# Optimization experiments

Hardware: AMD Instinct MI355X
Metric: run time of the kernel (lower is better)

## Reference

```python
import jax, jax.numpy as jnp
import numpy as np

LN_EPS = 1e-5
NEG_INF = -1e30


def setup_inputs() -> dict:
    key = jax.random.key(0)
    k_adj, k_feat, k_mask, k_w = jax.random.split(key, 4)
    B, N, H, R, L = 8, 400, 768, 46, 2
    adj = jax.random.uniform(k_adj, (B, N, N, R), dtype=jnp.float32)
    feature = jax.random.normal(k_feat, (B, N, H), dtype=jnp.float32)
    dmask = (jax.random.uniform(k_mask, (B, 1, N)) > 0.1).astype(jnp.float32)
    # per-layer, per-relation Linear(H, H, bias=False) weights, applied as x @ W
    W = jax.random.normal(k_w, (L, R, H, H), dtype=jnp.float32) / np.sqrt(H)
    return {"adj": adj, "feature": feature, "dmask": dmask, "W": W}


def reference(adj, feature, dmask, W):
    # adj: [B,N,N,R] -> [B,R,N,N]; dmask: [B,1,N] masks key/column axis
    B, N, _, R = adj.shape
    a = jnp.transpose(adj, (0, 3, 1, 2))           # [B,R,N,N]
    m = dmask[:, None, :, :]                        # [B,1,1,N]
    logits = a * m + (1.0 - m) * NEG_INF
    att = jax.nn.softmax(logits, axis=-1)           # [B,R,N,N] (layer-invariant)

    x = feature
    num_layers = W.shape[0]
    for layer in range(num_layers):
        # grouped per-relation linear: h[b,r,n,k] = feature[b,n,h] @ W[layer,r,h,k]
        h = jnp.einsum('bnh,rhk->brnk', x, W[layer])
        h = jax.nn.relu(jnp.einsum('brnm,brmk->brnk', att, h))
        addition = h.sum(axis=1)                    # sum over relations -> [B,N,H]
        z = jax.nn.relu(addition) / R
        # LayerNorm without affine params
        mu = jnp.mean(z, axis=-1, keepdims=True)
        var = jnp.var(z, axis=-1, keepdims=True)
        x = (z - mu) / jnp.sqrt(var + LN_EPS)
        # dropout is identity in eval mode
    return x
```

## Files before the change

### kernel.cpp

```cpp
#include <hip/hip_runtime.h>
#include <stdint.h>

#define BS 8
#define NN 400
#define HH 768
#define RR 46
#define MPAD 416
#define MFLAT2 3328
#define LDW2 3328
#define PADM 402

typedef _Float16 half8 __attribute__((ext_vector_type(8)));
typedef _Float16 half4v __attribute__((ext_vector_type(4)));
typedef float floatx4 __attribute__((ext_vector_type(4)));

__device__ __forceinline__ void async16(const void* g, void* l) {
  __builtin_amdgcn_global_load_lds((const __attribute__((address_space(1))) uint32_t*)g,
                                   (__attribute__((address_space(3))) uint32_t*)l, 16, 0, 0);
}

__device__ __forceinline__ int xcd_work(int flat, int nwg) {
  int q = nwg >> 3, rem = nwg & 7;
  int xcd = flat & 7, slot = flat >> 3;
  return (xcd < rem ? xcd * (q + 1) : rem * (q + 1) + (xcd - rem) * q) + slot;
}

__device__ __forceinline__ void vm_wait(int ahead) {
  if (ahead >= 2) asm volatile("s_waitcnt vmcnt(8)" ::: "memory");
  else if (ahead == 1) asm volatile("s_waitcnt vmcnt(4)" ::: "memory");
  else asm volatile("s_waitcnt vmcnt(0)" ::: "memory");
}
__device__ __forceinline__ void vm_wait2(int ahead) {
  if (ahead >= 2) asm volatile("s_waitcnt vmcnt(4)" ::: "memory");
  else if (ahead == 1) asm volatile("s_waitcnt vmcnt(2)" ::: "memory");
  else asm volatile("s_waitcnt vmcnt(0)" ::: "memory");
}
#define BAR_TOP() { __builtin_amdgcn_s_barrier(); __builtin_amdgcn_sched_barrier(0); }
#define BAR_BOT() { asm volatile("s_waitcnt lgkmcnt(0)" ::: "memory"); \
                    __builtin_amdgcn_s_barrier(); __builtin_amdgcn_sched_barrier(0); }
#define BAR_ONE() { asm volatile("s_barrier" ::: "memory"); __builtin_amdgcn_sched_barrier(0); }


__device__ __forceinline__ void stage_tile(const _Float16* __restrict__ g, int ld, int rowbase,
                                           int maxrow, int kbase, _Float16* lds, int t) {
  int w = t >> 6, lane = t & 63;
  int swz = ((lane & 3) ^ ((lane >> 3) & 3)) * 8;
#pragma unroll
  for (int j = 0; j < 2; ++j) {
    int chunk = w * 2 + j;
    int row = chunk * 16 + (lane >> 2);
    int grow = rowbase + row;
    grow = grow > maxrow ? maxrow : grow;
    async16(g + (size_t)grow * ld + kbase + swz, lds + chunk * 512);
  }
}

__device__ __forceinline__ void mma_tiles(const _Float16* As, const _Float16* Bs, int lane,
                                          int wr, int wc, floatx4 acc[4][4]) {
  int arow = wr + (lane & 15);
  int brow = wc + (lane & 15);
  int kswz = ((lane >> 4) ^ ((lane >> 1) & 3)) * 8;
  half8 a[4], b[4];
#pragma unroll
  for (int i = 0; i < 4; ++i) a[i] = *(const half8*)&As[(arow + i * 16) * 32 + kswz];
#pragma unroll
  for (int i = 0; i < 4; ++i) b[i] = *(const half8*)&Bs[(brow + i * 16) * 32 + kswz];
#pragma unroll
  for (int i = 0; i < 4; ++i)
#pragma unroll
    for (int j = 0; j < 4; ++j)
      acc[i][j] = __builtin_amdgcn_mfma_f32_16x16x32_f16(a[i], b[j], acc[i][j], 0, 0, 0);
}

__device__ __forceinline__ void mma8(const _Float16* As, const _Float16* Bs, int lane,
                                     int wr, int wc, floatx4 acc[4][2]) {
  int arow = wr + (lane & 15);
  int brow = wc + (lane & 15);
  int kswz = ((lane >> 4) ^ ((lane >> 1) & 3)) * 8;
  half8 a[4], b[2];
#pragma unroll
  for (int i = 0; i < 4; ++i) a[i] = *(const half8*)&As[(arow + i * 16) * 32 + kswz];
#pragma unroll
  for (int j = 0; j < 2; ++j) b[j] = *(const half8*)&Bs[(brow + j * 16) * 32 + kswz];
#pragma unroll
  for (int i = 0; i < 4; ++i)
#pragma unroll
    for (int j = 0; j < 2; ++j)
      acc[i][j] = __builtin_amdgcn_mfma_f32_16x16x32_f16(a[i], b[j], acc[i][j], 0, 0, 0);
}

__global__ __launch_bounds__(256) void conv_w(const float* __restrict__ W, _Float16* __restrict__ Wt) {
  __shared__ float tl[32][33];
  int t = threadIdx.x;
  int lr = blockIdx.y;
  int tr = blockIdx.x / 24, tc = blockIdx.x % 24;
  const float* src = W + (size_t)lr * HH * HH;
  _Float16* dst = Wt + (size_t)lr * HH * HH;
  int rl = t >> 5, cl = t & 31;
#pragma unroll
  for (int j = 0; j < 4; ++j)
    tl[rl + 8 * j][cl] = src[(size_t)(tr * 32 + rl + 8 * j) * HH + tc * 32 + cl];
  __syncthreads();
#pragma unroll
  for (int j = 0; j < 4; ++j)
    dst[(size_t)(tc * 32 + rl + 8 * j) * HH + tr * 32 + cl] = (_Float16)tl[cl][rl + 8 * j];
}

__global__ void conv_x(const float* __restrict__ f, _Float16* __restrict__ x16) {
  int i4 = blockIdx.x * 256 + threadIdx.x;
  int row = i4 / 192;
  int c4 = i4 - row * 192;
  int b = row / 416;
  int m = row - b * 416;
  half4v h = {};
  if (m < NN) {
    float4 v = *(const float4*)(f + ((size_t)(b * NN + m) * HH) + c4 * 4);
    h[0] = (_Float16)v.x; h[1] = (_Float16)v.y; h[2] = (_Float16)v.z; h[3] = (_Float16)v.w;
  }
  *(half4v*)&x16[(size_t)row * HH + c4 * 4] = h;
}

__global__ __launch_bounds__(512) void att_softmax(const float* __restrict__ adj,
                                                   const float* __restrict__ dmask,
                                                   _Float16* __restrict__ att) {
  __shared__ _Float16 sE[RR * PADM];
  __shared__ float sM[NN];
  int t = threadIdx.x;
  int n = blockIdx.x, b = blockIdx.y;
  const float4* src = (const float4*)(adj + ((size_t)b * NN + n) * NN * RR);
  for (int i = t; i < NN; i += 512) sM[i] = dmask[b * NN + i];
  float4 v[9];
#pragma unroll
  for (int k = 0; k < 9; ++k) {
    int idx = t + k * 512;
    if (idx < NN * RR / 4) v[k] = src[idx];
  }
  __syncthreads();
#pragma unroll
  for (int k = 0; k < 9; ++k) {
    int idx = t + k * 512;
    if (idx < NN * RR / 4) {
      int e0 = idx * 4;
      float vv[4] = {v[k].x, v[k].y, v[k].z, v[k].w};
#pragma unroll
      for (int j = 0; j < 4; ++j) {
        int e = e0 + j;
        int m = e / RR;
        int r = e - m * RR;
        float val = sM[m] > 0.5f ? __expf(vv[j]) : 0.0f;
        sE[r * PADM + m] = (_Float16)val;
      }
    }
  }
  __syncthreads();
  int lane = t & 63, wid = t >> 6;
  for (int r = wid; r < RR; r += 8) {
    const _Float16* row = &sE[r * PADM];
    float s = 0.f;
    for (int m = lane; m < NN; m += 64) s += (float)row[m];
#pragma unroll
    for (int o = 32; o; o >>= 1) s += __shfl_xor(s, o);
    float inv = 1.0f / s;
    _Float16* orow = att + (((size_t)b * RR + r) * NN + n) * MPAD;
    for (int m2 = lane * 2; m2 < MPAD; m2 += 128) {
      _Float16 lo = (_Float16)0.f, hi = (_Float16)0.f;
      if (m2 < NN) lo = (_Float16)((float)row[m2] * inv);
      if (m2 + 1 < NN) hi = (_Float16)((float)row[m2 + 1] * inv);
      union { _Float16 h[2]; uint32_t u; } pk;
      pk.h[0] = lo; pk.h[1] = hi;
      *(uint32_t*)&orow[m2] = pk.u;
    }
  }
}

__global__ __launch_bounds__(256) void gemm_xw(const _Float16* __restrict__ x16,
                                               const _Float16* __restrict__ Wt,
                                               _Float16* __restrict__ h1T, int layer, int r0, int rbase) {
  __shared__ __align__(16) char smraw[49152];
  int t = threadIdx.x;
  int work = xcd_work(blockIdx.x, gridDim.x);
  int r_i = work / 156;
  int rem = work - r_i * 156;
  int r = r0 + r_i;
  int mtile = rem / 6, ntile = rem % 6;
  const _Float16* A = x16;
  const _Float16* Bp = Wt + ((size_t)layer * RR + r) * HH * HH;
  int lane = t & 63, w = t >> 6;
  int wr = (w >> 1) * 64, wc = (w & 1) * 64;
  floatx4 acc[4][4] = {};
  stage_tile(A, HH, mtile * 128, MFLAT2 - 1, 0, (_Float16*)smraw, t);
  stage_tile(Bp, HH, ntile * 128, HH - 1, 0, (_Float16*)(smraw + 8192), t);
  stage_tile(A, HH, mtile * 128, MFLAT2 - 1, 32, (_Float16*)(smraw + 16384), t);
  stage_tile(Bp, HH, ntile * 128, HH - 1, 32, (_Float16*)(smraw + 24576), t);
  int cur = 0, stb = 2;
  for (int ks = 0; ks < 24; ++ks) {
    if (ks + 2 < 24) {
      char* nb = smraw + stb * 16384;
      stage_tile(A, HH, mtile * 128, MFLAT2 - 1, (ks + 2) * 32, (_Float16*)nb, t);
      stage_tile(Bp, HH, ntile * 128, HH - 1, (ks + 2) * 32, (_Float16*)(nb + 8192), t);
      stb = stb == 2 ? 0 : stb + 1;
    }
    vm_wait(ks + 2 < 24 ? 2 : (ks + 1 < 24 ? 1 : 0));
    BAR_TOP();
    char* cb = smraw + cur * 16384;
    mma_tiles((const _Float16*)cb, (const _Float16*)(cb + 8192), lane, wr, wc, acc);
    BAR_BOT();
    cur = cur == 2 ? 0 : cur + 1;
  }
  _Float16* outl = (_Float16*)smraw;
#pragma unroll
  for (int i = 0; i < 4; ++i) {
#pragma unroll
    for (int j = 0; j < 4; ++j) {
      int rl = wr + i * 16 + (lane >> 4) * 4;
      int cl = wc + j * 16 + (lane & 15);
      half4v v = {(_Float16)acc[i][j][0], (_Float16)acc[i][j][1],
                  (_Float16)acc[i][j][2], (_Float16)acc[i][j][3]};
      *(half4v*)&outl[cl * 136 + rl] = v;
    }
  }
  __syncthreads();
  _Float16* outp = h1T + (size_t)(r - rbase) * HH * LDW2;
#pragma unroll
  for (int pass = 0; pass < 8; ++pass) {
    int c = pass * 16 + (t >> 4);
    int ml = (t & 15) * 8;
    int gm = mtile * 128 + ml;
    int gn = ntile * 128 + c;
    half8 v = *(const half8*)&outl[c * 136 + ml];
    *(half8*)&outp[(size_t)gn * LDW2 + gm] = v;
  }
}

__global__ __launch_bounds__(512, 4) void gemm_att(const _Float16* __restrict__ att,
                                                   const _Float16* __restrict__ h1T,
                                                   float* __restrict__ partials, size_t psz,
                                                   int rs, int rcount, int rbase, int accflag,
                                                   int ngroups) {
  __shared__ __align__(16) char smraw[65536];
  int t = threadIdx.x;
  int work = xcd_work(blockIdx.x, gridDim.x);
  int ntile = work % 6;
  int tmp = work / 6;
  int mtile = tmp & 3; tmp >>= 2;
  int g = tmp % ngroups;
  int b = tmp / ngroups;
  int rbeg = rs + (g * rcount) / ngroups;
  int rend = rs + ((g + 1) * rcount) / ngroups;
  int nr = rend - rbeg;
  int total = nr * 13;
  float* part = partials + (size_t)g * psz;
  int lane = t & 63, w = t >> 6;
  int wr = (w >> 2) * 64, wc = (w & 3) * 32;
  floatx4 acc[4][2] = {}, sum[4][2] = {};

  int srow = w * 16 + (lane >> 2);
  int scol = ((lane & 3) ^ ((lane >> 3) & 3)) * 8;
  int ga = mtile * 128 + srow; ga = ga > NN - 1 ? NN - 1 : ga;
  int gb = ntile * 128 + srow;
  const _Float16* pa = att + ((size_t)b * RR + rbeg) * NN * MPAD + (size_t)ga * MPAD + scol;
  const _Float16* pb = h1T + (size_t)(rbeg - rbase) * HH * LDW2 + (size_t)gb * LDW2 + b * MPAD + scol;
  int nsk = 0;
  auto issue = [&](int buf) {
    char* lb = smraw + (buf << 14) + w * 1024;
    async16(pa, lb);
    async16(pb, lb + 8192);
    if (++nsk == 13) { nsk = 0; pa += (size_t)NN * MPAD - 384; pb += (size_t)HH * LDW2 - 384; }
    else { pa += 32; pb += 32; }
  };

  issue(0); issue(1); issue(2);
  vm_wait2(2);
  BAR_ONE();
  int cks = 0;
  for (int s = 0; s < total; ++s) {
    if (s + 3 < total) issue((s + 3) & 3);
    char* cb = smraw + ((s & 3) << 14);
    __builtin_amdgcn_s_setprio(1);
    mma8((const _Float16*)cb, (const _Float16*)(cb + 8192), lane, wr, wc, acc);
    __builtin_amdgcn_s_setprio(0);
    if (cks == 12) {
#pragma unroll
      for (int i = 0; i < 4; ++i)
#pragma unroll
        for (int j = 0; j < 2; ++j) {
#pragma unroll
          for (int q2 = 0; q2 < 4; ++q2) sum[i][j][q2] += fmaxf(acc[i][j][q2], 0.0f);
          acc[i][j] = (floatx4){0.f, 0.f, 0.f, 0.f};
        }
      cks = 0;
    } else ++cks;
    if (s + 1 < total) {
      int ahead = total - s - 2;
      vm_wait2(ahead > 2 ? 2 : ahead);
      BAR_ONE();
    }
  }
#pragma unroll
  for (int i = 0; i < 4; ++i) {
    int rl = wr + i * 16 + (lane >> 4) * 4;
    int grow = mtile * 128 + rl;
#pragma unroll
    for (int j = 0; j < 2; ++j) {
      int gcol = ntile * 128 + wc + j * 16 + (lane & 15);
#pragma unroll
      for (int q2 = 0; q2 < 4; ++q2) {
        if (grow + q2 < NN) {
          size_t idx = ((size_t)b * NN + grow + q2) * HH + gcol;
          float v = sum[i][j][q2];
          if (accflag) v += part[idx];
          part[idx] = v;
        }
      }
    }
  }
}

__global__ __launch_bounds__(256) void lnorm(const float* __restrict__ partials, size_t psz, int np,
                                             _Float16* __restrict__ x16, float* __restrict__ out) {
  int row = blockIdx.x;
  int t = threadIdx.x;
  int b = row / NN;
  int xrow = row + b * 16;
  float v[3];
  float s = 0.f, s2 = 0.f;
#pragma unroll
  for (int j = 0; j < 3; ++j) {
    float a = 0.f;
    for (int gidx = 0; gidx < np; ++gidx) a += partials[(size_t)gidx * psz + (size_t)row * HH + t + j * 256];
    v[j] = fmaxf(a, 0.f) * (1.0f / RR);
    s += v[j];
    s2 += v[j] * v[j];
  }
#pragma unroll
  for (int o = 32; o; o >>= 1) {
    s += __shfl_xor(s, o);
    s2 += __shfl_xor(s2, o);
  }
  __shared__ float rs_[4], rs2_[4];
  int lane = t & 63, wid = t >> 6;
  if (!lane) { rs_[wid] = s; rs2_[wid] = s2; }
  __syncthreads();
  s = rs_[0] + rs_[1] + rs_[2] + rs_[3];
  s2 = rs2_[0] + rs2_[1] + rs2_[2] + rs2_[3];
  float mu = s * (1.0f / HH);
  float var = s2 * (1.0f / HH) - mu * mu;
  float rstd = rsqrtf(var + 1e-5f);
#pragma unroll
  for (int j = 0; j < 3; ++j) {
    float o = (v[j] - mu) * rstd;
    out[(size_t)row * HH + t + j * 256] = o;
    x16[(size_t)xrow * HH + t + j * 256] = (_Float16)o;
  }
}

extern "C" void kernel_launch(void* const* d_in, const int* in_sizes, int n_in,
                              void* d_out, int out_size, void* d_ws, size_t ws_size,
                              hipStream_t stream) {
  const float* adj = (const float*)d_in[0];
  const float* feature = (const float*)d_in[1];
  const float* dmask = (const float*)d_in[2];
  const float* W = (const float*)d_in[3];
  float* out = (float*)d_out;

  uintptr_t base = (uintptr_t)d_ws;
  uintptr_t p = base;
  auto alloc = [&](size_t bytes) -> void* {
    uintptr_t q = (p + 255) & ~(uintptr_t)255;
    p = q + bytes;
    return (void*)q;
  };
  _Float16* att = (_Float16*)alloc((size_t)BS * RR * NN * MPAD * 2);
  _Float16* Wt = (_Float16*)alloc((size_t)2 * RR * HH * HH * 2);
  _Float16* x16 = (_Float16*)alloc((size_t)MFLAT2 * HH * 2);
  size_t psz = (size_t)(BS * NN) * HH;
  size_t pszB = psz * 4;
  size_t used = p - base;
  size_t rem = ws_size > used ? ws_size - used : 0;
  size_t perR = (size_t)HH * LDW2 * 2;
  size_t h1full = (size_t)RR * perR;

  conv_w<<<dim3(576, 2 * RR), 256, 0, stream>>>(W, Wt);
  conv_x<<<MFLAT2 * HH / 4 / 256, 256, 0, stream>>>(feature, x16);
  att_softmax<<<dim3(NN, BS), 512, 0, stream>>>(adj, dmask, att);

  if (rem >= h1full + 4 * pszB + 512) {
    _Float16* h1T = (_Float16*)alloc(h1full);
    int ngroups = (int)(((ws_size - (p - base)) - 256) / pszB);
    if (ngroups > 8) ngroups = 8;
    float* partials = (float*)alloc((size_t)ngroups * pszB);
    for (int layer = 0; layer < 2; ++layer) {
      gemm_xw<<<156 * RR, 256, 0, stream>>>(x16, Wt, h1T, layer, 0, 0);
      gemm_att<<<6 * 4 * ngroups * BS, 512, 0, stream>>>(att, h1T, partials, psz, 0, RR, 0, 0, ngroups);
      lnorm<<<BS * NN, 256, 0, stream>>>(partials, psz, ngroups, x16, out);
    }
  } else {
    float* partials = (float*)alloc(pszB);
    size_t rem2 = ws_size > (p - base) ? ws_size - (p - base) : 0;
    int RCmax = (int)(rem2 / perR);
    if (RCmax > RR) RCmax = RR;
    if (RCmax < 1) RCmax = 1;
    _Float16* h1T = (_Float16*)alloc((size_t)RCmax * perR);
    for (int layer = 0; layer < 2; ++layer) {
      for (int r0 = 0; r0 < RR; r0 += RCmax) {
        int rc = RR - r0 < RCmax ? RR - r0 : RCmax;
        gemm_xw<<<156 * rc, 256, 0, stream>>>(x16, Wt, h1T, layer, r0, r0);
        gemm_att<<<6 * 4 * 1 * BS, 512, 0, stream>>>(att, h1T, partials, psz, r0, rc, r0, r0 > 0, 1);
      }
      lnorm<<<BS * NN, 256, 0, stream>>>(partials, psz, 1, x16, out);
    }
  }
}
```

Before: 1.041 ms.

## Enlarge gemm_xw tiles to 256x256 with a 4-stage LDS pipeline

The per-relation x@W GEMM moves from 128x128 tiles with 256 threads to 256x256 tiles with 512 threads. Each wave now owns a 128x64 sub-tile, which doubles operand reuse per LDS load and halves the total global traffic for A and B. The triple-buffered loop with two barriers per k-step becomes a 4-deep async pipeline in 128KB of dynamic LDS, with one barrier per step and raised wave priority around the MFMAs. The epilogue does its transpose in a per-wave, XOR-swizzled LDS region to avoid bank conflicts. The cost is that only one block fits per CU, with higher register pressure and fewer blocks to spread across the GPU.

```diff
diff --git a/kernel.cpp b/kernel.cpp
--- a/kernel.cpp
+++ b/kernel.cpp
@@ -35,38 +35,21 @@
   else if (ahead == 1) asm volatile("s_waitcnt vmcnt(2)" ::: "memory");
   else asm volatile("s_waitcnt vmcnt(0)" ::: "memory");
 }
-#define BAR_TOP() { __builtin_amdgcn_s_barrier(); __builtin_amdgcn_sched_barrier(0); }
-#define BAR_BOT() { asm volatile("s_waitcnt lgkmcnt(0)" ::: "memory"); \
-                    __builtin_amdgcn_s_barrier(); __builtin_amdgcn_sched_barrier(0); }
 #define BAR_ONE() { asm volatile("s_barrier" ::: "memory"); __builtin_amdgcn_sched_barrier(0); }
 
 
-__device__ __forceinline__ void stage_tile(const _Float16* __restrict__ g, int ld, int rowbase,
-                                           int maxrow, int kbase, _Float16* lds, int t) {
-  int w = t >> 6, lane = t & 63;
-  int swz = ((lane & 3) ^ ((lane >> 3) & 3)) * 8;
-#pragma unroll
-  for (int j = 0; j < 2; ++j) {
-    int chunk = w * 2 + j;
-    int row = chunk * 16 + (lane >> 2);
-    int grow = rowbase + row;
-    grow = grow > maxrow ? maxrow : grow;
-    async16(g + (size_t)grow * ld + kbase + swz, lds + chunk * 512);
-  }
-}
-
-__device__ __forceinline__ void mma_tiles(const _Float16* As, const _Float16* Bs, int lane,
-                                          int wr, int wc, floatx4 acc[4][4]) {
+__device__ __forceinline__ void mma32(const _Float16* As, const _Float16* Bs, int lane,
+                                      int wr, int wc, floatx4 acc[8][4]) {
   int arow = wr + (lane & 15);
   int brow = wc + (lane & 15);
   int kswz = ((lane >> 4) ^ ((lane >> 1) & 3)) * 8;
-  half8 a[4], b[4];
-#pragma unroll
-  for (int i = 0; i < 4; ++i) a[i] = *(const half8*)&As[(arow + i * 16) * 32 + kswz];
-#pragma unroll
-  for (int i = 0; i < 4; ++i) b[i] = *(const half8*)&Bs[(brow + i * 16) * 32 + kswz];
-#pragma unroll
-  for (int i = 0; i < 4; ++i)
+  half8 a[8], b[4];
+#pragma unroll
+  for (int i = 0; i < 8; ++i) a[i] = *(const half8*)&As[(arow + i * 16) * 32 + kswz];
+#pragma unroll
+  for (int j = 0; j < 4; ++j) b[j] = *(const half8*)&Bs[(brow + j * 16) * 32 + kswz];
+#pragma unroll
+  for (int i = 0; i < 8; ++i)
 #pragma unroll
     for (int j = 0; j < 4; ++j)
       acc[i][j] = __builtin_amdgcn_mfma_f32_16x16x32_f16(a[i], b[j], acc[i][j], 0, 0, 0);
@@ -173,62 +156,79 @@
   }
 }
 
-__global__ __launch_bounds__(256) void gemm_xw(const _Float16* __restrict__ x16,
-                                               const _Float16* __restrict__ Wt,
-                                               _Float16* __restrict__ h1T, int layer, int r0, int rbase) {
-  __shared__ __align__(16) char smraw[49152];
+__global__ __launch_bounds__(512, 2) void gemm_xw(const _Float16* __restrict__ x16,
+                                                  const _Float16* __restrict__ Wt,
+                                                  _Float16* __restrict__ h1T, int layer, int r0, int rbase) {
+  extern __shared__ __align__(16) char smraw[];
   int t = threadIdx.x;
   int work = xcd_work(blockIdx.x, gridDim.x);
-  int r_i = work / 156;
-  int rem = work - r_i * 156;
+  int r_i = work / 39;
+  int rem = work - r_i * 39;
   int r = r0 + r_i;
-  int mtile = rem / 6, ntile = rem % 6;
-  const _Float16* A = x16;
+  int mtile = rem / 3, ntile = rem % 3;
   const _Float16* Bp = Wt + ((size_t)layer * RR + r) * HH * HH;
   int lane = t & 63, w = t >> 6;
-  int wr = (w >> 1) * 64, wc = (w & 1) * 64;
-  floatx4 acc[4][4] = {};
-  stage_tile(A, HH, mtile * 128, MFLAT2 - 1, 0, (_Float16*)smraw, t);
-  stage_tile(Bp, HH, ntile * 128, HH - 1, 0, (_Float16*)(smraw + 8192), t);
-  stage_tile(A, HH, mtile * 128, MFLAT2 - 1, 32, (_Float16*)(smraw + 16384), t);
-  stage_tile(Bp, HH, ntile * 128, HH - 1, 32, (_Float16*)(smraw + 24576), t);
-  int cur = 0, stb = 2;
-  for (int ks = 0; ks < 24; ++ks) {
-    if (ks + 2 < 24) {
-      char* nb = smraw + stb * 16384;
-      stage_tile(A, HH, mtile * 128, MFLAT2 - 1, (ks + 2) * 32, (_Float16*)nb, t);
-      stage_tile(Bp, HH, ntile * 128, HH - 1, (ks + 2) * 32, (_Float16*)(nb + 8192), t);
-      stb = stb == 2 ? 0 : stb + 1;
-    }
-    vm_wait(ks + 2 < 24 ? 2 : (ks + 1 < 24 ? 1 : 0));
-    BAR_TOP();
-    char* cb = smraw + cur * 16384;
-    mma_tiles((const _Float16*)cb, (const _Float16*)(cb + 8192), lane, wr, wc, acc);
-    BAR_BOT();
-    cur = cur == 2 ? 0 : cur + 1;
-  }
-  _Float16* outl = (_Float16*)smraw;
-#pragma unroll
-  for (int i = 0; i < 4; ++i) {
+  int wr = (w >> 2) * 128, wc = (w & 3) * 64;
+  floatx4 acc[8][4] = {};
+
+  int c0 = w * 2;
+  int swz = ((lane & 3) ^ ((lane >> 3) & 3)) * 8;
+  int ra0 = mtile * 256 + c0 * 16 + (lane >> 2);
+  int ra1 = ra0 + 16;
+  int rb0 = ntile * 256 + c0 * 16 + (lane >> 2);
+  int rb1 = rb0 + 16;
+  const _Float16* pa0 = x16 + (size_t)ra0 * HH + swz;
+  const _Float16* pa1 = x16 + (size_t)ra1 * HH + swz;
+  const _Float16* pb0 = Bp + (size_t)rb0 * HH + swz;
+  const _Float16* pb1 = Bp + (size_t)rb1 * HH + swz;
+  auto issue = [&](int buf) {
+    _Float16* lA = (_Float16*)(smraw + (buf << 15)) + c0 * 512;
+    _Float16* lB = (_Float16*)(smraw + (buf << 15) + 16384) + c0 * 512;
+    async16(pa0, lA); async16(pa1, lA + 512);
+    async16(pb0, lB); async16(pb1, lB + 512);
+    pa0 += 32; pa1 += 32; pb0 += 32; pb1 += 32;
+  };
+
+  issue(0); issue(1); issue(2);
+  vm_wait(2);
+  BAR_ONE();
+  for (int s = 0; s < 24; ++s) {
+    if (s + 3 < 24) issue((s + 3) & 3);
+    char* cb = smraw + ((s & 3) << 15);
+    __builtin_amdgcn_s_setprio(1);
+    mma32((const _Float16*)cb, (const _Float16*)(cb + 16384), lane, wr, wc, acc);
+    __builtin_amdgcn_s_setprio(0);
+    if (s + 1 < 24) {
+      int ahead = 24 - s - 2;
+      vm_wait(ahead > 2 ? 2 : ahead);
+      BAR_ONE();
+    }
+  }
+  __syncthreads();
+
+  _Float16* outl = (_Float16*)smraw + (size_t)w * 8192;
+#pragma unroll
+  for (int i = 0; i < 8; ++i) {
 #pragma unroll
     for (int j = 0; j < 4; ++j) {
-      int rl = wr + i * 16 + (lane >> 4) * 4;
-      int cl = wc + j * 16 + (lane & 15);
+      int rl = i * 16 + (lane >> 4) * 4;
+      int cl = j * 16 + (lane & 15);
+      int pos = rl ^ ((cl & 7) << 3);
       half4v v = {(_Float16)acc[i][j][0], (_Float16)acc[i][j][1],
                   (_Float16)acc[i][j][2], (_Float16)acc[i][j][3]};
-      *(half4v*)&outl[cl * 136 + rl] = v;
-    }
-  }
-  __syncthreads();
+      *(half4v*)&outl[cl * 128 + pos] = v;
+    }
+  }
   _Float16* outp = h1T + (size_t)(r - rbase) * HH * LDW2;
-#pragma unroll
-  for (int pass = 0; pass < 8; ++pass) {
-    int c = pass * 16 + (t >> 4);
-    int ml = (t & 15) * 8;
-    int gm = mtile * 128 + ml;
-    int gn = ntile * 128 + c;
-    half8 v = *(const half8*)&outl[c * 136 + ml];
-    *(half8*)&outp[(size_t)gn * LDW2 + gm] = v;
+  int gmb = mtile * 256 + wr;
+  int gnb = ntile * 256 + wc;
+#pragma unroll
+  for (int p = 0; p < 16; ++p) {
+    int c = p * 4 + (lane >> 4);
+    int mq = (lane & 15) * 8;
+    int mpos = mq ^ ((c & 7) << 3);
+    half8 v = *(const half8*)&outl[c * 128 + mpos];
+    *(half8*)&outp[(size_t)(gnb + c) * LDW2 + gmb + mq] = v;
   }
 }
 
@@ -363,6 +363,9 @@
   const float* W = (const float*)d_in[3];
   float* out = (float*)d_out;
 
+  (void)hipFuncSetAttribute((const void*)gemm_xw,
+                            hipFuncAttributeMaxDynamicSharedMemorySize, 131072);
+
   uintptr_t base = (uintptr_t)d_ws;
   uintptr_t p = base;
   auto alloc = [&](size_t bytes) -> void* {
@@ -390,7 +393,7 @@
     if (ngroups > 8) ngroups = 8;
     float* partials = (float*)alloc((size_t)ngroups * pszB);
     for (int layer = 0; layer < 2; ++layer) {
-      gemm_xw<<<156 * RR, 256, 0, stream>>>(x16, Wt, h1T, layer, 0, 0);
+      gemm_xw<<<39 * RR, 512, 131072, stream>>>(x16, Wt, h1T, layer, 0, 0);
       gemm_att<<<6 * 4 * ngroups * BS, 512, 0, stream>>>(att, h1T, partials, psz, 0, RR, 0, 0, ngroups);
       lnorm<<<BS * NN, 256, 0, stream>>>(partials, psz, ngroups, x16, out);
     }
@@ -404,7 +407,7 @@
     for (int layer = 0; layer < 2; ++layer) {
       for (int r0 = 0; r0 < RR; r0 += RCmax) {
         int rc = RR - r0 < RCmax ? RR - r0 : RCmax;
-        gemm_xw<<<156 * rc, 256, 0, stream>>>(x16, Wt, h1T, layer, r0, r0);
+        gemm_xw<<<39 * rc, 512, 131072, stream>>>(x16, Wt, h1T, layer, r0, r0);
         gemm_att<<<6 * 4 * 1 * BS, 512, 0, stream>>>(att, h1T, partials, psz, r0, rc, r0, r0 > 0, 1);
       }
       lnorm<<<BS * NN, 256, 0, stream>>>(partials, psz, 1, x16, out);
```

New measurement: 1.008 ms. 1.03x faster.
